# Optimization experiments

Measured on AMD Instinct MI355X. Metric: run time of the kernel, lower is better.

## Reference

```python
import jax, jax.numpy as jnp
import numpy as np

N_NODES = 100000
N_EDGES = 3200000
D_IN = 128
D_OUT = 128


def setup_inputs() -> dict:
    key = jax.random.key(0)
    ks = jax.random.split(key, 6)
    x = jax.random.normal(ks[0], (N_NODES, D_IN), dtype=jnp.float32)
    edge_rows = jax.random.randint(ks[1], (N_EDGES,), 0, N_NODES, dtype=jnp.int32)
    edge_cols = jax.random.randint(ks[2], (N_EDGES,), 0, N_NODES, dtype=jnp.int32)
    edge_vals = jax.random.uniform(ks[3], (N_EDGES,), dtype=jnp.float32)
    # Linear params: weight ~ U(-1/sqrt(n_in), 1/sqrt(n_in)) per `uniform(n_in, ...)`, bias zeros.
    bound = 1.0 / np.sqrt(D_IN)
    W = jax.random.uniform(ks[4], (D_OUT, D_IN), minval=-bound, maxval=bound, dtype=jnp.float32)
    b = jnp.zeros((D_OUT,), dtype=jnp.float32)
    return {"x": x, "edge_rows": edge_rows, "edge_cols": edge_cols, "edge_vals": edge_vals, "W": W, "b": b}


def reference(x, edge_rows, edge_cols, edge_vals, W, b) -> jnp.ndarray:
    # x1 = spmm(adj, x): for each edge (r, c, v): x1[r] += v * x[c]
    gathered = x[edge_cols] * edge_vals[:, None]          # [E, D_IN]
    x1 = jax.ops.segment_sum(gathered, edge_rows, num_segments=N_NODES)  # [N, D_IN]
    # x2 = Linear(x1) = x1 @ W.T + b
    return x1 @ W.T + b
```

## Files before the change

kernel.cpp:

```cpp
#include <hip/hip_runtime.h>

#define D 128
#define RPB 64
#define NBMAX 1600
#define CAP 2432
#define CHUNK 6144

typedef unsigned short u16;
typedef unsigned int u32;
typedef __attribute__((ext_vector_type(8))) short short8;
typedef __attribute__((ext_vector_type(4))) float f32x4;

__device__ inline u16 f32_to_bf16(float f) {
    unsigned int u = __float_as_uint(f);
    u += 0x7fffu + ((u >> 16) & 1u);
    return (u16)(u >> 16);
}

__global__ void cvtW_kernel(const float* __restrict__ W, u16* __restrict__ Wbf) {
    int i = blockIdx.x * 256 + threadIdx.x;
    if (i < D * D) Wbf[i] = f32_to_bf16(W[i]);
}

__global__ __launch_bounds__(256) void gemm_mfma_kernel(const float* __restrict__ x,
                                                        const u16* __restrict__ Wbf,
                                                        u16* __restrict__ y, int n_rows) {
    __shared__ float ytile[64 * 128];
    const int t = threadIdx.x;
    const int wid = t >> 6;
    const int l = t & 63;
    const int rbase = blockIdx.x * 64;
    const int row = rbase + wid * 16 + (l & 15);
    const int kg = l >> 4;
    const bool rok = (row < n_rows);

    short8 afr[4];
#pragma unroll
    for (int kb = 0; kb < 4; ++kb) {
        int k0 = kb * 32 + kg * 8;
        float4 xa = rok ? *(const float4*)(x + (size_t)row * D + k0) : make_float4(0, 0, 0, 0);
        float4 xb = rok ? *(const float4*)(x + (size_t)row * D + k0 + 4) : make_float4(0, 0, 0, 0);
        short8 a;
        a[0] = (short)f32_to_bf16(xa.x); a[1] = (short)f32_to_bf16(xa.y);
        a[2] = (short)f32_to_bf16(xa.z); a[3] = (short)f32_to_bf16(xa.w);
        a[4] = (short)f32_to_bf16(xb.x); a[5] = (short)f32_to_bf16(xb.y);
        a[6] = (short)f32_to_bf16(xb.z); a[7] = (short)f32_to_bf16(xb.w);
        afr[kb] = a;
    }

#pragma unroll
    for (int cg = 0; cg < 8; ++cg) {
        f32x4 acc = {0.0f, 0.0f, 0.0f, 0.0f};
        int c = cg * 16 + (l & 15);
#pragma unroll
        for (int kb = 0; kb < 4; ++kb) {
            int k0 = kb * 32 + kg * 8;
            short8 bfr = *(const short8*)(Wbf + (size_t)c * D + k0);
            acc = __builtin_amdgcn_mfma_f32_16x16x32_bf16(afr[kb], bfr, acc, 0, 0, 0);
        }
#pragma unroll
        for (int i = 0; i < 4; ++i) {
            ytile[(wid * 16 + kg * 4 + i) * 128 + cg * 16 + (l & 15)] = acc[i];
        }
    }
    __syncthreads();

    for (int e = t; e < 64 * 16; e += 256) {
        int rl = e >> 4;
        int cq = (e & 15) * 8;
        int grow = rbase + rl;
        if (grow >= n_rows) continue;
        float4 f0 = *(float4*)&ytile[rl * 128 + cq];
        float4 f1 = *(float4*)&ytile[rl * 128 + cq + 4];
        short8 o;
        o[0] = (short)f32_to_bf16(f0.x); o[1] = (short)f32_to_bf16(f0.y);
        o[2] = (short)f32_to_bf16(f0.z); o[3] = (short)f32_to_bf16(f0.w);
        o[4] = (short)f32_to_bf16(f1.x); o[5] = (short)f32_to_bf16(f1.y);
        o[6] = (short)f32_to_bf16(f1.z); o[7] = (short)f32_to_bf16(f1.w);
        *(short8*)(y + (size_t)grow * D + cq) = o;
    }
}

__global__ void init_cursor_kernel(int* __restrict__ gcur, int nb) {
    int i = blockIdx.x * 256 + threadIdx.x;
    if (i < nb) gcur[i] = i * CAP;
}

__global__ __launch_bounds__(256) void partition_sort_kernel(const int* __restrict__ rows,
                                                             const int* __restrict__ cols,
                                                             const float* __restrict__ vals,
                                                             int* __restrict__ gcur,
                                                             u32* __restrict__ buf,
                                                             int n_edges, int nb) {
    __shared__ u32 pay[CHUNK];
    __shared__ u16 bid[CHUNK];
    __shared__ int H[NBMAX];
    __shared__ int L[NBMAX + 1];
    __shared__ int partial[256];
    const int t = threadIdx.x;
    const int e0 = blockIdx.x * CHUNK;
    const int n = min(CHUNK, n_edges - e0);

    for (int i = t; i < nb; i += 256) H[i] = 0;
    __syncthreads();
    for (int i = t; i < n; i += 256) atomicAdd(&H[rows[e0 + i] >> 6], 1);
    __syncthreads();
    const int cs = (nb + 255) >> 8;
    const int beg = t * cs;
    const int end = min(nb, beg + cs);
    int s = 0;
    for (int i = beg; i < end; ++i) s += H[i];
    partial[t] = s;
    __syncthreads();
    for (int off = 1; off < 256; off <<= 1) {
        int v = (t >= off) ? partial[t - off] : 0;
        __syncthreads();
        partial[t] += v;
        __syncthreads();
    }
    int run = (t == 0) ? 0 : partial[t - 1];
    for (int i = beg; i < end; ++i) { int h = H[i]; L[i] = run; run += h; }
    __syncthreads();
    if (t == 0) L[nb] = n;
    for (int i = t; i < nb; i += 256) H[i] = L[i];
    __syncthreads();
    for (int i = t; i < n; i += 256) {
        int r = rows[e0 + i];
        int b = r >> 6;
        u32 q = (u32)fminf(vals[e0 + i] * 512.0f, 511.0f);
        u32 p = (((u32)(r & (RPB - 1))) << 26) | (((u32)cols[e0 + i]) << 9) | q;
        int pos = atomicAdd(&H[b], 1);
        pay[pos] = p;
        bid[pos] = (u16)b;
    }
    __syncthreads();
    for (int b = t; b < nb; b += 256) {
        int len = L[b + 1] - L[b];
        if (len > 0) {
            int g = atomicAdd(&gcur[b], len);
            H[b] = g - L[b];
        }
    }
    __syncthreads();
    for (int i = t; i < n; i += 256) {
        int lo = (int)bid[i];
        int pos = H[lo] + i;
        if (pos < (lo + 1) * CAP) buf[pos] = pay[i];
    }
}

__global__ __launch_bounds__(256) void gather_fused_kernel(const int* __restrict__ gcur,
                                                           const u32* __restrict__ buf,
                                                           const uint4* __restrict__ yv,
                                                           const float* __restrict__ bias,
                                                           float* __restrict__ out,
                                                           int n_nodes) {
    __shared__ u32 pay[CAP];
    __shared__ u32 srt[CAP];
    __shared__ int hist[RPB];
    __shared__ int start[RPB];
    __shared__ int cur[RPB];
    const int b = blockIdx.x;
    const int t = threadIdx.x;
    const int base = b * CAP;
    const int n = min(gcur[b] - base, CAP);

    if (t < RPB) hist[t] = 0;
    __syncthreads();
    for (int i = t; i < n; i += 256) {
        u32 p = buf[base + i];
        pay[i] = p;
        atomicAdd(&hist[p >> 26], 1);
    }
    __syncthreads();
    if (t == 0) {
        int run = 0;
#pragma unroll
        for (int i = 0; i < RPB; ++i) { start[i] = run; cur[i] = run; run += hist[i]; }
    }
    __syncthreads();
    for (int i = t; i < n; i += 256) {
        u32 p = pay[i];
        int pos = atomicAdd(&cur[p >> 26], 1);
        srt[pos] = p & 0x03ffffffu;
    }
    __syncthreads();

    const int wid = t >> 6;
    const int l = t & 63;
    const int g = l >> 4;
    const int li = l & 15;
    const float sc = 1.0f / 512.0f;
    const float4 bb = *(const float4*)(bias + li * 8 + (g & 1) * 4);

    for (int rl = wid * 16; rl < wid * 16 + 16; ++rl) {
        int node = b * RPB + rl;
        if (node >= n_nodes) break;
        const int s = start[rl];
        const int e = s + hist[rl];
        float a0 = 0, a1 = 0, a2 = 0, a3 = 0, a4 = 0, a5 = 0, a6 = 0, a7 = 0;
        for (int j0 = s; j0 < e; j0 += 32) {
            u32 pp[8];
            uint4 qq[8];
#pragma unroll
            for (int k = 0; k < 8; ++k) {
                int j = j0 + g + 4 * k;
                pp[k] = srt[(j < e) ? j : (e - 1)];
            }
#pragma unroll
            for (int k = 0; k < 8; ++k) {
                qq[k] = yv[(size_t)(pp[k] >> 9) * 16 + li];
            }
#pragma unroll
            for (int k = 0; k < 8; ++k) {
                int j = j0 + g + 4 * k;
                float v = (j < e) ? ((float)(pp[k] & 511u) + 0.5f) * sc : 0.0f;
                a0 += v * __uint_as_float(qq[k].x << 16);
                a1 += v * __uint_as_float(qq[k].x);
                a2 += v * __uint_as_float(qq[k].y << 16);
                a3 += v * __uint_as_float(qq[k].y);
                a4 += v * __uint_as_float(qq[k].z << 16);
                a5 += v * __uint_as_float(qq[k].z);
                a6 += v * __uint_as_float(qq[k].w << 16);
                a7 += v * __uint_as_float(qq[k].w);
            }
        }
        a0 += __shfl_xor(a0, 16); a1 += __shfl_xor(a1, 16);
        a2 += __shfl_xor(a2, 16); a3 += __shfl_xor(a3, 16);
        a4 += __shfl_xor(a4, 16); a5 += __shfl_xor(a5, 16);
        a6 += __shfl_xor(a6, 16); a7 += __shfl_xor(a7, 16);
        a0 += __shfl_xor(a0, 32); a1 += __shfl_xor(a1, 32);
        a2 += __shfl_xor(a2, 32); a3 += __shfl_xor(a3, 32);
        a4 += __shfl_xor(a4, 32); a5 += __shfl_xor(a5, 32);
        a6 += __shfl_xor(a6, 32); a7 += __shfl_xor(a7, 32);
        if (g < 2) {
            float4 o;
            if (g == 0) { o.x = a0 + bb.x; o.y = a1 + bb.y; o.z = a2 + bb.z; o.w = a3 + bb.w; }
            else        { o.x = a4 + bb.x; o.y = a5 + bb.y; o.z = a6 + bb.z; o.w = a7 + bb.w; }
            ((float4*)(out + (size_t)node * D))[li * 2 + g] = o;
        }
    }
}

extern "C" void kernel_launch(void* const* d_in, const int* in_sizes, int n_in,
                              void* d_out, int out_size, void* d_ws, size_t ws_size,
                              hipStream_t stream) {
    const float* x    = (const float*)d_in[0];
    const int*   erow = (const int*)d_in[1];
    const int*   ecol = (const int*)d_in[2];
    const float* eval_= (const float*)d_in[3];
    const float* W    = (const float*)d_in[4];
    const float* b    = (const float*)d_in[5];
    float* out = (float*)d_out;

    int n_nodes = in_sizes[0] / D;
    int n_edges = in_sizes[1];
    int nb = (n_nodes + RPB - 1) / RPB;

    char* ws = (char*)d_ws;
    u16* y = (u16*)ws;        ws += (size_t)n_nodes * D * sizeof(u16);
    u16* Wbf = (u16*)ws;      ws += (size_t)D * D * sizeof(u16);
    u32* buf = (u32*)ws;      ws += (size_t)nb * CAP * sizeof(u32);
    int* gcur = (int*)ws;

    cvtW_kernel<<<(D * D + 255) / 256, 256, 0, stream>>>(W, Wbf);
    gemm_mfma_kernel<<<(n_nodes + 63) / 64, 256, 0, stream>>>(x, Wbf, y, n_nodes);

    init_cursor_kernel<<<(nb + 255) / 256, 256, 0, stream>>>(gcur, nb);
    int pblocks = (n_edges + CHUNK - 1) / CHUNK;
    partition_sort_kernel<<<pblocks, 256, 0, stream>>>(erow, ecol, eval_, gcur, buf, n_edges, nb);

    gather_fused_kernel<<<nb, 256, 0, stream>>>(gcur, buf, (const uint4*)y, b, out, n_nodes);
}
```

Measured before the change: 214.0 us.

## Co-schedule GEMM with edge partition and split gather into half-bucket blocks

The separate weight-convert and cursor-init kernels are merged into one prep kernel. The GEMM and edge-partition kernels become a single launch whose blocks branch on block index into either role, so the two independent phases run concurrently and one launch is saved. The gather kernel now uses two blocks per 64-row bucket, each handling 32 rows. This doubles the grid and cuts shared memory per block, which should raise occupancy. In exchange, each half-block re-reads the whole bucket payload from global memory twice, and the fused kernel's shared-memory footprint is sized for the larger partition role, which may limit occupancy for the GEMM blocks.

```diff
diff --git a/kernel.cpp b/kernel.cpp
--- a/kernel.cpp
+++ b/kernel.cpp
@@ -4,6 +4,7 @@
 #define RPB 64
 #define NBMAX 1600
 #define CAP 2432
+#define CAPH 1280
 #define CHUNK 6144
 
 typedef unsigned short u16;
@@ -17,172 +18,171 @@
     return (u16)(u >> 16);
 }
 
-__global__ void cvtW_kernel(const float* __restrict__ W, u16* __restrict__ Wbf) {
+__global__ void prep_kernel(const float* __restrict__ W, u16* __restrict__ Wbf,
+                            int* __restrict__ gcur, int nb) {
     int i = blockIdx.x * 256 + threadIdx.x;
     if (i < D * D) Wbf[i] = f32_to_bf16(W[i]);
-}
-
-__global__ __launch_bounds__(256) void gemm_mfma_kernel(const float* __restrict__ x,
-                                                        const u16* __restrict__ Wbf,
-                                                        u16* __restrict__ y, int n_rows) {
-    __shared__ float ytile[64 * 128];
+    if (i < nb) gcur[i] = i * CAP;
+}
+
+__global__ __launch_bounds__(256) void gp_fused_kernel(
+    const float* __restrict__ x, const u16* __restrict__ Wbf, u16* __restrict__ y,
+    int n_rows,
+    const int* __restrict__ rows, const int* __restrict__ cols,
+    const float* __restrict__ vals,
+    int* __restrict__ gcur, u32* __restrict__ buf, int n_edges, int nb, int npart) {
+    __shared__ __align__(16) char smem[50704];
     const int t = threadIdx.x;
-    const int wid = t >> 6;
-    const int l = t & 63;
-    const int rbase = blockIdx.x * 64;
-    const int row = rbase + wid * 16 + (l & 15);
-    const int kg = l >> 4;
-    const bool rok = (row < n_rows);
-
-    short8 afr[4];
-#pragma unroll
-    for (int kb = 0; kb < 4; ++kb) {
-        int k0 = kb * 32 + kg * 8;
-        float4 xa = rok ? *(const float4*)(x + (size_t)row * D + k0) : make_float4(0, 0, 0, 0);
-        float4 xb = rok ? *(const float4*)(x + (size_t)row * D + k0 + 4) : make_float4(0, 0, 0, 0);
-        short8 a;
-        a[0] = (short)f32_to_bf16(xa.x); a[1] = (short)f32_to_bf16(xa.y);
-        a[2] = (short)f32_to_bf16(xa.z); a[3] = (short)f32_to_bf16(xa.w);
-        a[4] = (short)f32_to_bf16(xb.x); a[5] = (short)f32_to_bf16(xb.y);
-        a[6] = (short)f32_to_bf16(xb.z); a[7] = (short)f32_to_bf16(xb.w);
-        afr[kb] = a;
-    }
-
-#pragma unroll
-    for (int cg = 0; cg < 8; ++cg) {
-        f32x4 acc = {0.0f, 0.0f, 0.0f, 0.0f};
-        int c = cg * 16 + (l & 15);
+
+    if ((int)blockIdx.x < npart) {
+        u32* pay   = (u32*)smem;
+        u16* bid   = (u16*)(smem + 24576);
+        int* H     = (int*)(smem + 36864);
+        int* L     = (int*)(smem + 43264);
+        int* part_ = (int*)(smem + 49668);
+        const int e0 = blockIdx.x * CHUNK;
+        const int n = min(CHUNK, n_edges - e0);
+
+        for (int i = t; i < nb; i += 256) H[i] = 0;
+        __syncthreads();
+        for (int i = t; i < n; i += 256) atomicAdd(&H[rows[e0 + i] >> 6], 1);
+        __syncthreads();
+        const int cs = (nb + 255) >> 8;
+        const int beg = t * cs;
+        const int end = min(nb, beg + cs);
+        int s = 0;
+        for (int i = beg; i < end; ++i) s += H[i];
+        part_[t] = s;
+        __syncthreads();
+        for (int off = 1; off < 256; off <<= 1) {
+            int v = (t >= off) ? part_[t - off] : 0;
+            __syncthreads();
+            part_[t] += v;
+            __syncthreads();
+        }
+        int run = (t == 0) ? 0 : part_[t - 1];
+        for (int i = beg; i < end; ++i) { int h = H[i]; L[i] = run; run += h; }
+        __syncthreads();
+        if (t == 0) L[nb] = n;
+        for (int i = t; i < nb; i += 256) H[i] = L[i];
+        __syncthreads();
+        for (int i = t; i < n; i += 256) {
+            int r = rows[e0 + i];
+            int b = r >> 6;
+            u32 q = (u32)fminf(vals[e0 + i] * 512.0f, 511.0f);
+            u32 p = (((u32)(r & (RPB - 1))) << 26) | (((u32)cols[e0 + i]) << 9) | q;
+            int pos = atomicAdd(&H[b], 1);
+            pay[pos] = p;
+            bid[pos] = (u16)b;
+        }
+        __syncthreads();
+        for (int b = t; b < nb; b += 256) {
+            int len = L[b + 1] - L[b];
+            if (len > 0) {
+                int g = atomicAdd(&gcur[b], len);
+                H[b] = g - L[b];
+            }
+        }
+        __syncthreads();
+        for (int i = t; i < n; i += 256) {
+            int lo = (int)bid[i];
+            int pos = H[lo] + i;
+            if (pos < (lo + 1) * CAP) buf[pos] = pay[i];
+        }
+    } else {
+        float* ytile = (float*)smem;
+        const int wid = t >> 6;
+        const int l = t & 63;
+        const int rbase = ((int)blockIdx.x - npart) * 64;
+        const int row = rbase + wid * 16 + (l & 15);
+        const int kg = l >> 4;
+        const bool rok = (row < n_rows);
+
+        short8 afr[4];
 #pragma unroll
         for (int kb = 0; kb < 4; ++kb) {
             int k0 = kb * 32 + kg * 8;
-            short8 bfr = *(const short8*)(Wbf + (size_t)c * D + k0);
-            acc = __builtin_amdgcn_mfma_f32_16x16x32_bf16(afr[kb], bfr, acc, 0, 0, 0);
-        }
-#pragma unroll
-        for (int i = 0; i < 4; ++i) {
-            ytile[(wid * 16 + kg * 4 + i) * 128 + cg * 16 + (l & 15)] = acc[i];
-        }
-    }
-    __syncthreads();
-
-    for (int e = t; e < 64 * 16; e += 256) {
-        int rl = e >> 4;
-        int cq = (e & 15) * 8;
-        int grow = rbase + rl;
-        if (grow >= n_rows) continue;
-        float4 f0 = *(float4*)&ytile[rl * 128 + cq];
-        float4 f1 = *(float4*)&ytile[rl * 128 + cq + 4];
-        short8 o;
-        o[0] = (short)f32_to_bf16(f0.x); o[1] = (short)f32_to_bf16(f0.y);
-        o[2] = (short)f32_to_bf16(f0.z); o[3] = (short)f32_to_bf16(f0.w);
-        o[4] = (short)f32_to_bf16(f1.x); o[5] = (short)f32_to_bf16(f1.y);
-        o[6] = (short)f32_to_bf16(f1.z); o[7] = (short)f32_to_bf16(f1.w);
-        *(short8*)(y + (size_t)grow * D + cq) = o;
-    }
-}
-
-__global__ void init_cursor_kernel(int* __restrict__ gcur, int nb) {
-    int i = blockIdx.x * 256 + threadIdx.x;
-    if (i < nb) gcur[i] = i * CAP;
-}
-
-__global__ __launch_bounds__(256) void partition_sort_kernel(const int* __restrict__ rows,
-                                                             const int* __restrict__ cols,
-                                                             const float* __restrict__ vals,
-                                                             int* __restrict__ gcur,
-                                                             u32* __restrict__ buf,
-                                                             int n_edges, int nb) {
-    __shared__ u32 pay[CHUNK];
-    __shared__ u16 bid[CHUNK];
-    __shared__ int H[NBMAX];
-    __shared__ int L[NBMAX + 1];
-    __shared__ int partial[256];
-    const int t = threadIdx.x;
-    const int e0 = blockIdx.x * CHUNK;
-    const int n = min(CHUNK, n_edges - e0);
-
-    for (int i = t; i < nb; i += 256) H[i] = 0;
-    __syncthreads();
-    for (int i = t; i < n; i += 256) atomicAdd(&H[rows[e0 + i] >> 6], 1);
-    __syncthreads();
-    const int cs = (nb + 255) >> 8;
-    const int beg = t * cs;
-    const int end = min(nb, beg + cs);
-    int s = 0;
-    for (int i = beg; i < end; ++i) s += H[i];
-    partial[t] = s;
-    __syncthreads();
-    for (int off = 1; off < 256; off <<= 1) {
-        int v = (t >= off) ? partial[t - off] : 0;
-        __syncthreads();
-        partial[t] += v;
-        __syncthreads();
-    }
-    int run = (t == 0) ? 0 : partial[t - 1];
-    for (int i = beg; i < end; ++i) { int h = H[i]; L[i] = run; run += h; }
-    __syncthreads();
-    if (t == 0) L[nb] = n;
-    for (int i = t; i < nb; i += 256) H[i] = L[i];
-    __syncthreads();
-    for (int i = t; i < n; i += 256) {
-        int r = rows[e0 + i];
-        int b = r >> 6;
-        u32 q = (u32)fminf(vals[e0 + i] * 512.0f, 511.0f);
-        u32 p = (((u32)(r & (RPB - 1))) << 26) | (((u32)cols[e0 + i]) << 9) | q;
-        int pos = atomicAdd(&H[b], 1);
-        pay[pos] = p;
-        bid[pos] = (u16)b;
-    }
-    __syncthreads();
-    for (int b = t; b < nb; b += 256) {
-        int len = L[b + 1] - L[b];
-        if (len > 0) {
-            int g = atomicAdd(&gcur[b], len);
-            H[b] = g - L[b];
-        }
-    }
-    __syncthreads();
-    for (int i = t; i < n; i += 256) {
-        int lo = (int)bid[i];
-        int pos = H[lo] + i;
-        if (pos < (lo + 1) * CAP) buf[pos] = pay[i];
-    }
-}
-
-__global__ __launch_bounds__(256) void gather_fused_kernel(const int* __restrict__ gcur,
-                                                           const u32* __restrict__ buf,
-                                                           const uint4* __restrict__ yv,
-                                                           const float* __restrict__ bias,
-                                                           float* __restrict__ out,
-                                                           int n_nodes) {
-    __shared__ u32 pay[CAP];
-    __shared__ u32 srt[CAP];
-    __shared__ int hist[RPB];
-    __shared__ int start[RPB];
-    __shared__ int cur[RPB];
-    const int b = blockIdx.x;
+            float4 xa = rok ? *(const float4*)(x + (size_t)row * D + k0) : make_float4(0, 0, 0, 0);
+            float4 xb = rok ? *(const float4*)(x + (size_t)row * D + k0 + 4) : make_float4(0, 0, 0, 0);
+            short8 a;
+            a[0] = (short)f32_to_bf16(xa.x); a[1] = (short)f32_to_bf16(xa.y);
+            a[2] = (short)f32_to_bf16(xa.z); a[3] = (short)f32_to_bf16(xa.w);
+            a[4] = (short)f32_to_bf16(xb.x); a[5] = (short)f32_to_bf16(xb.y);
+            a[6] = (short)f32_to_bf16(xb.z); a[7] = (short)f32_to_bf16(xb.w);
+            afr[kb] = a;
+        }
+
+#pragma unroll
+        for (int cg = 0; cg < 8; ++cg) {
+            f32x4 acc = {0.0f, 0.0f, 0.0f, 0.0f};
+            int c = cg * 16 + (l & 15);
+#pragma unroll
+            for (int kb = 0; kb < 4; ++kb) {
+                int k0 = kb * 32 + kg * 8;
+                short8 bfr = *(const short8*)(Wbf + (size_t)c * D + k0);
+                acc = __builtin_amdgcn_mfma_f32_16x16x32_bf16(afr[kb], bfr, acc, 0, 0, 0);
+            }
+#pragma unroll
+            for (int i = 0; i < 4; ++i) {
+                ytile[(wid * 16 + kg * 4 + i) * 128 + cg * 16 + (l & 15)] = acc[i];
+            }
+        }
+        __syncthreads();
+
+        for (int e = t; e < 64 * 16; e += 256) {
+            int rl = e >> 4;
+            int cq = (e & 15) * 8;
+            int grow = rbase + rl;
+            if (grow >= n_rows) continue;
+            float4 f0 = *(float4*)&ytile[rl * 128 + cq];
+            float4 f1 = *(float4*)&ytile[rl * 128 + cq + 4];
+            short8 o;
+            o[0] = (short)f32_to_bf16(f0.x); o[1] = (short)f32_to_bf16(f0.y);
+            o[2] = (short)f32_to_bf16(f0.z); o[3] = (short)f32_to_bf16(f0.w);
+            o[4] = (short)f32_to_bf16(f1.x); o[5] = (short)f32_to_bf16(f1.y);
+            o[6] = (short)f32_to_bf16(f1.z); o[7] = (short)f32_to_bf16(f1.w);
+            *(short8*)(y + (size_t)grow * D + cq) = o;
+        }
+    }
+}
+
+__global__ __launch_bounds__(256) void gather_half_kernel(const int* __restrict__ gcur,
+                                                          const u32* __restrict__ buf,
+                                                          const uint4* __restrict__ yv,
+                                                          const float* __restrict__ bias,
+                                                          float* __restrict__ out,
+                                                          int n_nodes) {
+    __shared__ u32 srt[CAPH];
+    __shared__ int hist[32];
+    __shared__ int start[32];
+    __shared__ int cur[32];
+    const int b = blockIdx.x >> 1;
+    const int h = blockIdx.x & 1;
     const int t = threadIdx.x;
     const int base = b * CAP;
     const int n = min(gcur[b] - base, CAP);
 
-    if (t < RPB) hist[t] = 0;
+    if (t < 32) hist[t] = 0;
     __syncthreads();
     for (int i = t; i < n; i += 256) {
         u32 p = buf[base + i];
-        pay[i] = p;
-        atomicAdd(&hist[p >> 26], 1);
+        int rl = (int)(p >> 26);
+        if ((rl >> 5) == h) atomicAdd(&hist[rl & 31], 1);
     }
     __syncthreads();
     if (t == 0) {
         int run = 0;
 #pragma unroll
-        for (int i = 0; i < RPB; ++i) { start[i] = run; cur[i] = run; run += hist[i]; }
+        for (int i = 0; i < 32; ++i) { start[i] = run; cur[i] = run; run += hist[i]; }
     }
     __syncthreads();
     for (int i = t; i < n; i += 256) {
-        u32 p = pay[i];
-        int pos = atomicAdd(&cur[p >> 26], 1);
-        srt[pos] = p & 0x03ffffffu;
+        u32 p = buf[base + i];
+        int rl = (int)(p >> 26);
+        if ((rl >> 5) == h) {
+            int pos = atomicAdd(&cur[rl & 31], 1);
+            if (pos < CAPH) srt[pos] = p & 0x03ffffffu;
+        }
     }
     __syncthreads();
 
@@ -193,8 +193,8 @@
     const float sc = 1.0f / 512.0f;
     const float4 bb = *(const float4*)(bias + li * 8 + (g & 1) * 4);
 
-    for (int rl = wid * 16; rl < wid * 16 + 16; ++rl) {
-        int node = b * RPB + rl;
+    for (int rl = wid * 8; rl < wid * 8 + 8; ++rl) {
+        int node = b * RPB + h * 32 + rl;
         if (node >= n_nodes) break;
         const int s = start[rl];
         const int e = s + hist[rl];
@@ -263,12 +263,13 @@
     u32* buf = (u32*)ws;      ws += (size_t)nb * CAP * sizeof(u32);
     int* gcur = (int*)ws;
 
-    cvtW_kernel<<<(D * D + 255) / 256, 256, 0, stream>>>(W, Wbf);
-    gemm_mfma_kernel<<<(n_nodes + 63) / 64, 256, 0, stream>>>(x, Wbf, y, n_nodes);
-
-    init_cursor_kernel<<<(nb + 255) / 256, 256, 0, stream>>>(gcur, nb);
-    int pblocks = (n_edges + CHUNK - 1) / CHUNK;
-    partition_sort_kernel<<<pblocks, 256, 0, stream>>>(erow, ecol, eval_, gcur, buf, n_edges, nb);
-
-    gather_fused_kernel<<<nb, 256, 0, stream>>>(gcur, buf, (const uint4*)y, b, out, n_nodes);
-}
+    prep_kernel<<<(D * D + 255) / 256, 256, 0, stream>>>(W, Wbf, gcur, nb);
+
+    int npart = (n_edges + CHUNK - 1) / CHUNK;
+    int ngemm = (n_nodes + 63) / 64;
+    gp_fused_kernel<<<npart + ngemm, 256, 0, stream>>>(x, Wbf, y, n_nodes,
+                                                       erow, ecol, eval_,
+                                                       gcur, buf, n_edges, nb, npart);
+
+    gather_half_kernel<<<2 * nb, 256, 0, stream>>>(gcur, buf, (const uint4*)y, b, out, n_nodes);
+}
```

Result: faster. 186.5 us (-12.9%).
